# Kernel optimization log

Hardware: AMD Instinct MI355X
Metric: run time of the kernel (lower is better)

## Reference

```python
import jax, jax.numpy as jnp
import numpy as np

NUM_LEARNERS = 50000
NUM_SCENES = 2000
EMBED_DIM = 128
SPARSITY = 0.1


def setup_inputs() -> dict:
    key = jax.random.key(0)
    k_m, k_w1, k_b1, k_w2, k_b2 = jax.random.split(key, 5)
    m = jax.random.uniform(k_m, (NUM_LEARNERS, NUM_SCENES), dtype=jnp.float32)
    m = jnp.where(m < SPARSITY, m, 0.0)
    return {
        "normalized_matrix": m,
        "W1": jax.random.normal(k_w1, (1, 16), dtype=jnp.float32),
        "b1": jax.random.normal(k_b1, (16,), dtype=jnp.float32),
        "W2": jax.random.normal(k_w2, (16, EMBED_DIM), dtype=jnp.float32),
        "b2": jax.random.normal(k_b2, (EMBED_DIM,), dtype=jnp.float32),
    }


def reference(normalized_matrix, W1, b1, W2, b2):
    # The torch module feeds the nonzero COLUMN INDICES (as floats) of each row
    # into MLP(1->16->d) and mean-pools. Since the MLP input is just the index j,
    # precompute mlp_out[j] for all scenes once, then a masked matmul + count
    # division gives the per-row mean over nonzero positions.
    num_scenes = normalized_matrix.shape[1]
    idx = jnp.arange(num_scenes, dtype=normalized_matrix.dtype)[:, None]  # [S, 1]
    h = jax.nn.relu(idx @ W1 + b1)                                        # [S, 16]
    mlp_out = h @ W2 + b2                                                 # [S, d]

    mask = (normalized_matrix != 0).astype(normalized_matrix.dtype)       # [L, S]
    counts = mask.sum(axis=1, keepdims=True)                              # [L, 1]
    # rows with zero nonzeros yield an all-zero mask row -> zero embedding,
    # matching the torch zeros fallback; clamp denominator to avoid 0/0.
    emb = (mask @ mlp_out) / jnp.maximum(counts, 1.0)                     # [L, d]
    return emb
```

## Files before the change

kernel.cpp:

```cpp
#include <hip/hip_runtime.h>

#define NUM_LEARNERS 50000
#define NUM_SCENES   2000
#define EMBED_DIM    128
#define HID          16

__global__ __launch_bounds__(256) void fused_gather_mean_kernel(
    const float* __restrict__ M,
    const float* __restrict__ W1, const float* __restrict__ b1,
    const float* __restrict__ W2, const float* __restrict__ b2,
    float* __restrict__ out)
{
    __shared__ unsigned short idxbuf[4][2048];
    const int  wave = threadIdx.x >> 6;
    const int  lane = threadIdx.x & 63;
    const long row  = (long)blockIdx.x * 4 + wave;

    const int g   = lane >> 2;
    const int sub = lane & 3;
    float w1v[4], b1v[4];
#pragma unroll
    for (int c = 0; c < 4; ++c) {
        w1v[c] = W1[4 * sub + c];
        b1v[c] = b1[4 * sub + c];
    }

    const float4* __restrict__ M4 = (const float4*)(M + row * NUM_SCENES);
    unsigned short* myidx = idxbuf[wave];

    float4 v[8];
#pragma unroll
    for (int it = 0; it < 8; ++it) {
        int c4 = it * 64 + lane;
        if (c4 < 500) v[it] = M4[c4];
        else          v[it] = make_float4(0.f, 0.f, 0.f, 0.f);
    }

    int count = 0;
#pragma unroll
    for (int it = 0; it < 8; ++it) {
        int c4 = it * 64 + lane;
        float vals[4] = {v[it].x, v[it].y, v[it].z, v[it].w};
#pragma unroll
        for (int c = 0; c < 4; ++c) {
            bool nz = (vals[c] != 0.0f);
            unsigned long long m = __ballot(nz);
            if (nz) {
                int below = __builtin_amdgcn_mbcnt_hi(
                    (unsigned)(m >> 32),
                    __builtin_amdgcn_mbcnt_lo((unsigned)m, 0));
                myidx[count + below] = (unsigned short)(c4 * 4 + c);
            }
            count += __popcll(m);
        }
    }

    __syncthreads();

    float4 acc = make_float4(0.f, 0.f, 0.f, 0.f);
    const int nIter = (count + 63) >> 6;
    for (int t = 0; t < nIter; ++t) {
        int base = t * 64 + g * 4;
        ushort4 idx4 = *(const ushort4*)&myidx[base];
        const unsigned short* iq = (const unsigned short*)&idx4;
#pragma unroll
        for (int q = 0; q < 4; ++q) {
            float x    = (float)iq[q];
            float mval = (base + q < count) ? 1.0f : 0.0f;
#pragma unroll
            for (int c = 0; c < 4; ++c) {
                float h = fmaxf(fmaf(x, w1v[c], b1v[c]), 0.0f);
                (&acc.x)[c] = fmaf(h, mval, (&acc.x)[c]);
            }
        }
    }

#pragma unroll
    for (int off = 4; off < 64; off <<= 1) {
        acc.x += __shfl_xor(acc.x, off);
        acc.y += __shfl_xor(acc.y, off);
        acc.z += __shfl_xor(acc.z, off);
        acc.w += __shfl_xor(acc.w, off);
    }
    float s[HID];
#pragma unroll
    for (int a = 0; a < 4; ++a) {
        s[4 * a + 0] = __shfl(acc.x, a);
        s[4 * a + 1] = __shfl(acc.y, a);
        s[4 * a + 2] = __shfl(acc.z, a);
        s[4 * a + 3] = __shfl(acc.w, a);
    }

    const float cnt = (float)count;
    const float inv = 1.0f / fmaxf(cnt, 1.0f);
    const float2* __restrict__ W2v = (const float2*)W2;
    float2 bv = ((const float2*)b2)[lane];
    float e0 = cnt * bv.x;
    float e1 = cnt * bv.y;
#pragma unroll
    for (int k = 0; k < HID; ++k) {
        float2 w = W2v[k * 64 + lane];
        e0 = fmaf(s[k], w.x, e0);
        e1 = fmaf(s[k], w.y, e1);
    }
    ((float2*)out)[row * 64 + lane] = make_float2(e0 * inv, e1 * inv);
}

extern "C" void kernel_launch(void* const* d_in, const int* in_sizes, int n_in,
                              void* d_out, int out_size, void* d_ws, size_t ws_size,
                              hipStream_t stream) {
    const float* M  = (const float*)d_in[0];
    const float* W1 = (const float*)d_in[1];
    const float* b1 = (const float*)d_in[2];
    const float* W2 = (const float*)d_in[3];
    const float* b2 = (const float*)d_in[4];
    float* out = (float*)d_out;

    fused_gather_mean_kernel<<<NUM_LEARNERS / 4, 256, 0, stream>>>(
        M, W1, b1, W2, b2, out);
}
```

Measured before the change: 521.4 us.

## Replace ballot-compaction gather with bf16 MFMA masked matmul over hidden activations

Instead of compacting nonzero column indices into LDS and looping over them, each wave now handles 16 rows. It builds bf16 mask fragments and recomputes the hidden ReLU activations per column block, then accumulates the hidden sums and the nonzero counts with 16x16x32 MFMA instructions. Row loads are software-pipelined four stages deep and the LDS staging and barrier are gone. The cost is computing the hidden activations for every column, not only the nonzero ones. It also rounds those activations to bf16, which can reduce accuracy.

```diff
diff --git a/kernel.cpp b/kernel.cpp
--- a/kernel.cpp
+++ b/kernel.cpp
@@ -5,105 +5,139 @@
 #define EMBED_DIM    128
 #define HID          16
 
-__global__ __launch_bounds__(256) void fused_gather_mean_kernel(
+typedef __attribute__((ext_vector_type(8))) short bf16x8;
+typedef __attribute__((ext_vector_type(4))) float f32x4;
+
+union FragU { unsigned int u[4]; bf16x8 v; };
+
+__global__ __launch_bounds__(64, 4) void fused_gather_mean_kernel(
     const float* __restrict__ M,
     const float* __restrict__ W1, const float* __restrict__ b1,
     const float* __restrict__ W2, const float* __restrict__ b2,
     float* __restrict__ out)
 {
-    __shared__ unsigned short idxbuf[4][2048];
-    const int  wave = threadIdx.x >> 6;
-    const int  lane = threadIdx.x & 63;
-    const long row  = (long)blockIdx.x * 4 + wave;
+    const int lane = threadIdx.x & 63;
+    const int r    = lane & 15;
+    const int g    = lane >> 4;
 
-    const int g   = lane >> 2;
-    const int sub = lane & 3;
-    float w1v[4], b1v[4];
+    const long row0 = (long)blockIdx.x * 16;
+    const float* __restrict__ mrow = M + (row0 + r) * NUM_SCENES;
+
+    const float w1r = W1[r];
+    const float b1r = b1[r];
+
+    f32x4 acc_s = {0.f, 0.f, 0.f, 0.f};
+    f32x4 acc_c = {0.f, 0.f, 0.f, 0.f};
+
+    FragU ones;
+    ones.u[0] = 0x3F803F80u; ones.u[1] = 0x3F803F80u;
+    ones.u[2] = 0x3F803F80u; ones.u[3] = 0x3F803F80u;
+
+    float4 ld_lo[4], ld_hi[4];
+
+    auto issue = [&](int t, int slot) {
+        int kb = t * 32 + 8 * g;
+        kb = (kb > 1992) ? 1992 : kb;
+        const float4* p = (const float4*)(mrow + kb);
+        ld_lo[slot] = p[0];
+        ld_hi[slot] = p[1];
+    };
+
+    auto step = [&](int t, int slot, bool tail) {
+        float va[8];
+        va[0] = ld_lo[slot].x; va[1] = ld_lo[slot].y;
+        va[2] = ld_lo[slot].z; va[3] = ld_lo[slot].w;
+        va[4] = ld_hi[slot].x; va[5] = ld_hi[slot].y;
+        va[6] = ld_hi[slot].z; va[7] = ld_hi[slot].w;
+
+        FragU mf;
 #pragma unroll
-    for (int c = 0; c < 4; ++c) {
-        w1v[c] = W1[4 * sub + c];
-        b1v[c] = b1[4 * sub + c];
+        for (int m = 0; m < 4; ++m) {
+            unsigned int l_ = (va[2 * m]     != 0.0f) ? 0x00003F80u : 0u;
+            unsigned int h_ = (va[2 * m + 1] != 0.0f) ? 0x3F800000u : 0u;
+            mf.u[m] = l_ | h_;
+        }
+        if (tail) {
+            unsigned int keep = (g < 2) ? 0xFFFFFFFFu : 0u;
+#pragma unroll
+            for (int m = 0; m < 4; ++m) mf.u[m] &= keep;
+        }
+
+        const float kbase = (float)(t * 32 + 8 * g);
+        FragU hf;
+#pragma unroll
+        for (int m = 0; m < 4; ++m) {
+            float h0 = fmaxf(fmaf(kbase + (float)(2 * m),     w1r, b1r), 0.0f);
+            float h1 = fmaxf(fmaf(kbase + (float)(2 * m + 1), w1r, b1r), 0.0f);
+            unsigned int pk;
+            asm("v_cvt_pk_bf16_f32 %0, %1, %2" : "=v"(pk) : "v"(h0), "v"(h1));
+            hf.u[m] = pk;
+        }
+
+        acc_s = __builtin_amdgcn_mfma_f32_16x16x32_bf16(hf.v,   mf.v, acc_s, 0, 0, 0);
+        acc_c = __builtin_amdgcn_mfma_f32_16x16x32_bf16(ones.v, mf.v, acc_c, 0, 0, 0);
+    };
+
+#pragma unroll
+    for (int t = 0; t < 4; ++t) issue(t, t);
+
+#pragma unroll 4
+    for (int t = 0; t < 60; ++t) {
+        step(t, t & 3, false);
+        issue(t + 4, t & 3);
+    }
+    step(60, 0, false);
+    step(61, 1, false);
+    step(62, 2, true);
+
+    float sg_[4][4];
+#pragma unroll
+    for (int q = 0; q < 4; ++q) sg_[0][q] = acc_s[q];
+#pragma unroll
+    for (int q = 0; q < 4; ++q) sg_[1][q] = __shfl_xor(sg_[0][q], 16);
+#pragma unroll
+    for (int q = 0; q < 4; ++q) sg_[2][q] = __shfl_xor(sg_[0][q], 32);
+#pragma unroll
+    for (int q = 0; q < 4; ++q) sg_[3][q] = __shfl_xor(sg_[1][q], 32);
+
+    const float cnt = acc_c[0];
+    const float inv = 1.0f / fmaxf(cnt, 1.0f);
+
+    float4 e[8];
+    const float4* b2v = (const float4*)(b2 + 32 * g);
+#pragma unroll
+    for (int u = 0; u < 8; ++u) {
+        float4 b = b2v[u];
+        e[u].x = cnt * b.x; e[u].y = cnt * b.y;
+        e[u].z = cnt * b.z; e[u].w = cnt * b.w;
     }
 
-    const float4* __restrict__ M4 = (const float4*)(M + row * NUM_SCENES);
-    unsigned short* myidx = idxbuf[wave];
-
-    float4 v[8];
 #pragma unroll
-    for (int it = 0; it < 8; ++it) {
-        int c4 = it * 64 + lane;
-        if (c4 < 500) v[it] = M4[c4];
-        else          v[it] = make_float4(0.f, 0.f, 0.f, 0.f);
-    }
-
-    int count = 0;
-#pragma unroll
-    for (int it = 0; it < 8; ++it) {
-        int c4 = it * 64 + lane;
-        float vals[4] = {v[it].x, v[it].y, v[it].z, v[it].w};
-#pragma unroll
-        for (int c = 0; c < 4; ++c) {
-            bool nz = (vals[c] != 0.0f);
-            unsigned long long m = __ballot(nz);
-            if (nz) {
-                int below = __builtin_amdgcn_mbcnt_hi(
-                    (unsigned)(m >> 32),
-                    __builtin_amdgcn_mbcnt_lo((unsigned)m, 0));
-                myidx[count + below] = (unsigned short)(c4 * 4 + c);
-            }
-            count += __popcll(m);
-        }
-    }
-
-    __syncthreads();
-
-    float4 acc = make_float4(0.f, 0.f, 0.f, 0.f);
-    const int nIter = (count + 63) >> 6;
-    for (int t = 0; t < nIter; ++t) {
-        int base = t * 64 + g * 4;
-        ushort4 idx4 = *(const ushort4*)&myidx[base];
-        const unsigned short* iq = (const unsigned short*)&idx4;
+    for (int i = 0; i < 4; ++i) {
+        const int kk = 4 * (g ^ i);
 #pragma unroll
         for (int q = 0; q < 4; ++q) {
-            float x    = (float)iq[q];
-            float mval = (base + q < count) ? 1.0f : 0.0f;
+            const float sval = sg_[i][q];
+            const float4* w2p = (const float4*)(W2 + (kk + q) * EMBED_DIM + 32 * g);
 #pragma unroll
-            for (int c = 0; c < 4; ++c) {
-                float h = fmaxf(fmaf(x, w1v[c], b1v[c]), 0.0f);
-                (&acc.x)[c] = fmaf(h, mval, (&acc.x)[c]);
+            for (int u = 0; u < 8; ++u) {
+                float4 w = w2p[u];
+                e[u].x = fmaf(sval, w.x, e[u].x);
+                e[u].y = fmaf(sval, w.y, e[u].y);
+                e[u].z = fmaf(sval, w.z, e[u].z);
+                e[u].w = fmaf(sval, w.w, e[u].w);
             }
         }
     }
 
+    float4* op = (float4*)(out + (row0 + r) * EMBED_DIM + 32 * g);
 #pragma unroll
-    for (int off = 4; off < 64; off <<= 1) {
-        acc.x += __shfl_xor(acc.x, off);
-        acc.y += __shfl_xor(acc.y, off);
-        acc.z += __shfl_xor(acc.z, off);
-        acc.w += __shfl_xor(acc.w, off);
+    for (int u = 0; u < 8; ++u) {
+        float4 o;
+        o.x = e[u].x * inv; o.y = e[u].y * inv;
+        o.z = e[u].z * inv; o.w = e[u].w * inv;
+        op[u] = o;
     }
-    float s[HID];
-#pragma unroll
-    for (int a = 0; a < 4; ++a) {
-        s[4 * a + 0] = __shfl(acc.x, a);
-        s[4 * a + 1] = __shfl(acc.y, a);
-        s[4 * a + 2] = __shfl(acc.z, a);
-        s[4 * a + 3] = __shfl(acc.w, a);
-    }
-
-    const float cnt = (float)count;
-    const float inv = 1.0f / fmaxf(cnt, 1.0f);
-    const float2* __restrict__ W2v = (const float2*)W2;
-    float2 bv = ((const float2*)b2)[lane];
-    float e0 = cnt * bv.x;
-    float e1 = cnt * bv.y;
-#pragma unroll
-    for (int k = 0; k < HID; ++k) {
-        float2 w = W2v[k * 64 + lane];
-        e0 = fmaf(s[k], w.x, e0);
-        e1 = fmaf(s[k], w.y, e1);
-    }
-    ((float2*)out)[row * 64 + lane] = make_float2(e0 * inv, e1 * inv);
 }
 
 extern "C" void kernel_launch(void* const* d_in, const int* in_sizes, int n_in,
@@ -116,6 +150,6 @@
     const float* b2 = (const float*)d_in[4];
     float* out = (float*)d_out;
 
-    fused_gather_mean_kernel<<<NUM_LEARNERS / 4, 256, 0, stream>>>(
+    fused_gather_mean_kernel<<<NUM_LEARNERS / 16, 64, 0, stream>>>(
         M, W1, b1, W2, b2, out);
 }
```

Result: slower. 545.0 us (+4.5%).
